# Performance work log

Hardware: AMD Instinct MI355X
Metric: run time of the kernel (lower is better)

The kernel has to match this reference:

```python
import jax, jax.numpy as jnp
import numpy as np

U, G, I, D = 10000, 3000, 8000, 32
LAYERS, SOCIAL_LAYERS = 3, 2
NNZ_UI, NNZ_GI = 720000, 440000
L_MEM = 20
B = 4096


def setup_inputs() -> dict:
    key = jax.random.key(0)
    ks = jax.random.split(key, 24)
    s_u = 1.0 / np.sqrt(U).astype(np.float32)
    s_i = 1.0 / np.sqrt(I).astype(np.float32)
    return {
        "group_inputs": jax.random.randint(ks[0], (B,), 0, G, dtype=jnp.int32),
        "item_inputs": jax.random.randint(ks[1], (B,), 0, I, dtype=jnp.int32),
        "user_emb": jax.random.normal(ks[2], (U, D), jnp.float32) * 0.1,
        "group_emb": jax.random.normal(ks[3], (G, D), jnp.float32) * 0.1,
        "item_emb": jax.random.normal(ks[4], (I, D), jnp.float32) * 0.1,
        "ui_rows": jax.random.randint(ks[5], (NNZ_UI,), 0, U + I, dtype=jnp.int32),
        "ui_cols": jax.random.randint(ks[6], (NNZ_UI,), 0, U + I, dtype=jnp.int32),
        "ui_vals": jax.random.uniform(ks[7], (NNZ_UI,), jnp.float32) * 0.02,
        "gi_rows": jax.random.randint(ks[8], (NNZ_GI,), 0, G + I, dtype=jnp.int32),
        "gi_cols": jax.random.randint(ks[9], (NNZ_GI,), 0, G + I, dtype=jnp.int32),
        "gi_vals": jax.random.uniform(ks[10], (NNZ_GI,), jnp.float32) * 0.02,
        "overlap_user": jax.random.normal(ks[11], (U, U), jnp.float32) * (0.1 * s_u),
        "overlap_item": jax.random.normal(ks[12], (I, I), jnp.float32) * (0.1 * s_i),
        "all_group_users": jax.random.randint(ks[13], (G, L_MEM), 0, U, dtype=jnp.int32),
        "all_group_mask": jax.random.uniform(ks[14], (G, L_MEM), jnp.float32) / L_MEM,
        "gate_w1": jax.random.normal(ks[15], (D, D), jnp.float32) * 0.1,
        "gate_b1": jnp.zeros((D,), jnp.float32),
        "gate_w2": jax.random.normal(ks[16], (D, 1), jnp.float32) * 0.1,
        "gate_b2": jnp.zeros((1,), jnp.float32),
        "pred_w1": jax.random.normal(ks[17], (D, 8), jnp.float32) * 0.1,
        "pred_b1": jnp.zeros((8,), jnp.float32),
        "pred_w2": jax.random.normal(ks[18], (8, 1), jnp.float32) * 0.1,
        "pred_b2": jnp.zeros((1,), jnp.float32),
    }


def _spmm(rows, cols, vals, x, n):
    # COO sparse-dense matmul: out[r] += vals * x[c]
    return jax.ops.segment_sum(vals[:, None] * x[cols], rows, num_segments=n)


def reference(group_inputs, item_inputs, user_emb, group_emb, item_emb,
              ui_rows, ui_cols, ui_vals, gi_rows, gi_cols, gi_vals,
              overlap_user, overlap_item, all_group_users, all_group_mask,
              gate_w1, gate_b1, gate_w2, gate_b2,
              pred_w1, pred_b1, pred_w2, pred_b2):
    # ---- GraphConvolution: user-item propagation ----
    ui = jnp.concatenate([user_emb, item_emb])           # [U+I, D]
    embs_ui = [ui]
    for _ in range(LAYERS):
        ui = _spmm(ui_rows, ui_cols, ui_vals, ui, U + I)
        embs_ui.append(ui)
    user_layers = [e[:U] for e in embs_ui]
    item_layers = [e[U:] for e in embs_ui]
    user_emb_for_user = jnp.mean(jnp.stack(user_layers, 1), axis=1)   # [U, D]
    item_emb_for_user = jnp.mean(jnp.stack(item_layers, 1), axis=1)   # [I, D]

    # ---- group-item propagation ----
    gi = jnp.concatenate([group_emb, item_emb_for_user])  # [G+I, D]
    embs_gi = [gi]
    for _ in range(LAYERS):
        gi = _spmm(gi_rows, gi_cols, gi_vals, gi, G + I)
        embs_gi.append(gi)
    group_gi = [e[:G] for e in embs_gi]
    item_gi = [e[G:] for e in embs_gi]
    i_emb = jnp.mean(jnp.stack(item_gi, 1), axis=1)       # [I, D]

    g_layers = []
    for i in range(LAYERS + 1):
        if i % 2 == 0:
            g_layers.append(group_gi[i])
        else:
            emb_in = jnp.concatenate([group_emb, item_layers[i - 1]])
            g_layers.append(_spmm(gi_rows, gi_cols, gi_vals, emb_in, G + I)[:G])
    g_emb = jnp.mean(jnp.stack(g_layers, 1), axis=1)      # [G, D]

    # ---- SocialRelationshipAgg (dense power-series + gathered pooling) ----
    ue = user_emb_for_user
    acc = ue
    for _ in range(SOCIAL_LAYERS):
        ue = overlap_user @ ue
        acc = acc + ue
    members = acc[all_group_users]                        # [G, L, D]
    group_userlayer = jnp.einsum('gl,gld->gd', all_group_mask, members)

    # ---- Gate ----
    x = jnp.concatenate([g_emb, group_userlayer])         # [2G, D]
    h = jax.nn.relu(x @ gate_w1 + gate_b1)
    w = jax.nn.sigmoid(h @ gate_w2 + gate_b2)             # [2G, 1]
    group_final = w[:G] * g_emb + w[G:] * group_userlayer

    # ---- OverlapGraphConvolution on items ----
    it = i_emb
    iacc = it
    for _ in range(SOCIAL_LAYERS):
        it = overlap_item @ it
        iacc = iacc + it

    # ---- Predict ----
    ge = group_final[group_inputs]                        # [B, D]
    ie = iacc[item_inputs]                                # [B, D]
    p = jax.nn.relu((ge * ie) @ pred_w1 + pred_b1)
    return jax.nn.sigmoid(p @ pred_w2 + pred_b2)          # [B, 1]
```

## Files before the change

### kernel.cpp

```cpp
#include <hip/hip_runtime.h>
#include <math.h>

#define U_N 10000
#define G_N 3000
#define I_N 8000
#define D_N 32
#define NNZ_UI 720000
#define NNZ_GI 440000
#define L_MEM 20
#define B_N 4096
#define UI_N (U_N + I_N)
#define GI_N (G_N + I_N)
#define CAP 128
#define KSPLIT 8

static __host__ int cdiv(int a, int b) { return (a + b - 1) / b; }

typedef __attribute__((ext_vector_type(8))) short bf16x8;
typedef __attribute__((ext_vector_type(4))) float f32x4;

__device__ __forceinline__ short f32_to_bf16(float f) {
    unsigned u = __float_as_uint(f);
    unsigned r = (u + 0x7FFFu + ((u >> 16) & 1u)) >> 16;
    return (short)r;
}


__global__ __launch_bounds__(256) void bucket_fill(const int* __restrict__ rows,
                                                   const int* __restrict__ cols,
                                                   const float* __restrict__ vals,
                                                   int nnz, int* __restrict__ cnt,
                                                   int2* __restrict__ bkt) {
    int i = blockIdx.x * 256 + threadIdx.x;
    if (i >= nnz) return;
    int r = rows[i];
    int pos = atomicAdd(&cnt[r], 1);
    if (pos < CAP) {
        int2 e; e.x = cols[i]; e.y = __float_as_int(vals[i]);
        bkt[(size_t)r * CAP + pos] = e;
    }
}

__global__ __launch_bounds__(256) void spmm_split(const int* __restrict__ cnt,
                                                  const int2* __restrict__ bkt,
                                                  const float* __restrict__ x1,
                                                  const float* __restrict__ x2,
                                                  int split,
                                                  float* __restrict__ out, int nrows) {
    int row = blockIdx.x * 8 + (threadIdx.x >> 5);
    if (row >= nrows) return;
    int d = threadIdx.x & 31;
    int deg = cnt[row];
    if (deg > CAP) deg = CAP;
    const int2* bk = bkt + (size_t)row * CAP;
    float acc = 0.f;
    int j = 0;
#define GATHER(e) ((e.x < split) ? x1[(size_t)e.x * 32 + d] \
                                 : x2[(size_t)(e.x - split) * 32 + d])
    for (; j + 3 < deg; j += 4) {
        int2 e0 = bk[j], e1 = bk[j + 1], e2 = bk[j + 2], e3 = bk[j + 3];
        float g0 = GATHER(e0), g1 = GATHER(e1), g2 = GATHER(e2), g3 = GATHER(e3);
        acc = fmaf(__int_as_float(e0.y), g0, acc);
        acc = fmaf(__int_as_float(e1.y), g1, acc);
        acc = fmaf(__int_as_float(e2.y), g2, acc);
        acc = fmaf(__int_as_float(e3.y), g3, acc);
    }
    for (; j < deg; ++j) {
        int2 e = bk[j];
        acc = fmaf(__int_as_float(e.y), GATHER(e), acc);
    }
#undef GATHER
    out[(size_t)row * 32 + d] = acc;
}


__global__ __launch_bounds__(256) void mean_ui(const float* __restrict__ uemb,
                                               const float* __restrict__ iemb0,
                                               const float* __restrict__ ui1,
                                               const float* __restrict__ ui2,
                                               const float* __restrict__ ui3,
                                               float* __restrict__ uefu,
                                               float* __restrict__ accu,
                                               float* __restrict__ iefu) {
    int idx = blockIdx.x * 256 + threadIdx.x;
    if (idx >= UI_N * 32) return;
    const int UOFF = U_N * 32;
    float base = (idx < UOFF) ? uemb[idx] : iemb0[idx - UOFF];
    float m = 0.25f * (base + ui1[idx] + ui2[idx] + ui3[idx]);
    if (idx < UOFF) { uefu[idx] = m; accu[idx] = m; }
    else iefu[idx - UOFF] = m;
}

__global__ __launch_bounds__(256) void mean_gi_items(const float* __restrict__ iefu,
                                                     const float* __restrict__ gi1,
                                                     const float* __restrict__ gi2,
                                                     const float* __restrict__ gi3,
                                                     float* __restrict__ iemb,
                                                     float* __restrict__ iacc) {
    int idx = blockIdx.x * 256 + threadIdx.x;
    if (idx >= I_N * 32) return;
    const int GOFF = G_N * 32;
    float m = 0.25f * (iefu[idx] + gi1[GOFF + idx] + gi2[GOFF + idx] + gi3[GOFF + idx]);
    iemb[idx] = m;
    iacc[idx] = m;
}

__global__ __launch_bounds__(256) void mean_g(const float* __restrict__ gemb0,
                                              const float* __restrict__ gt1,
                                              const float* __restrict__ gi2,
                                              const float* __restrict__ gt3,
                                              float* __restrict__ gemb) {
    int idx = blockIdx.x * 256 + threadIdx.x;
    if (idx >= G_N * 32) return;
    gemb[idx] = 0.25f * (gemb0[idx] + gt1[idx] + gi2[idx] + gt3[idx]);
}


__global__ __launch_bounds__(256) void pack_xb(const float* __restrict__ x,
                                               short* __restrict__ XB, int N, int ktiles) {
    int idx = blockIdx.x * 256 + threadIdx.x;
    int total = ktiles * 2 * 64;
    if (idx >= total) return;
    int lane = idx & 63;
    int th = idx >> 6;
    int h = th & 1;
    int t = th >> 1;
    int q = lane >> 4;
    int n = (lane & 15) + h * 16;
    short v[8];
#pragma unroll
    for (int j = 0; j < 8; ++j) {
        int c = t * 32 + q * 8 + j;
        v[j] = (c < N) ? f32_to_bf16(x[(size_t)c * 32 + n]) : (short)0;
    }
    short* dst = XB + (size_t)idx * 8;
#pragma unroll
    for (int j = 0; j < 8; ++j) dst[j] = v[j];
}

__global__ __launch_bounds__(256) void dense_mfma(const float* __restrict__ A,
                                                  const short* __restrict__ XB,
                                                  float* __restrict__ out,
                                                  float* __restrict__ out2,
                                                  int N, int ktiles) {
    int wid = (blockIdx.x * 256 + threadIdx.x) >> 6;
    int lane = threadIdx.x & 63;
    int strips = N >> 4;
    int strip = wid / KSPLIT;
    int ks = wid - strip * KSPLIT;
    if (strip >= strips) return;
    int r0 = strip << 4;
    int m = lane & 15;
    int q = lane >> 4;
    const float* arow = A + (size_t)(r0 + m) * N + q * 8;
    const bf16x8* xb = (const bf16x8*)XB;
    f32x4 acc0 = {0.f, 0.f, 0.f, 0.f};
    f32x4 acc1 = {0.f, 0.f, 0.f, 0.f};
    for (int t = ks; t < ktiles; t += KSPLIT) {
        int c0 = t * 32;
        bf16x8 afrag;
        if (c0 + 32 <= N) {
            float4 lo = *(const float4*)(arow + c0);
            float4 hi = *(const float4*)(arow + c0 + 4);
            afrag[0] = f32_to_bf16(lo.x); afrag[1] = f32_to_bf16(lo.y);
            afrag[2] = f32_to_bf16(lo.z); afrag[3] = f32_to_bf16(lo.w);
            afrag[4] = f32_to_bf16(hi.x); afrag[5] = f32_to_bf16(hi.y);
            afrag[6] = f32_to_bf16(hi.z); afrag[7] = f32_to_bf16(hi.w);
        } else {
#pragma unroll
            for (int j = 0; j < 8; ++j) {
                int c = c0 + q * 8 + j;
                afrag[j] = (c < N) ? f32_to_bf16(arow[c0 + j]) : (short)0;
            }
        }
        bf16x8 b0 = xb[(size_t)(t * 2 + 0) * 64 + lane];
        bf16x8 b1 = xb[(size_t)(t * 2 + 1) * 64 + lane];
        acc0 = __builtin_amdgcn_mfma_f32_16x16x32_bf16(afrag, b0, acc0, 0, 0, 0);
        acc1 = __builtin_amdgcn_mfma_f32_16x16x32_bf16(afrag, b1, acc1, 0, 0, 0);
    }
#pragma unroll
    for (int i = 0; i < 4; ++i) {
        size_t o = (size_t)(r0 + q * 4 + i) * 32 + m;
        atomicAdd(&out[o], acc0[i]);
        atomicAdd(&out[o + 16], acc1[i]);
        if (out2) {
            atomicAdd(&out2[o], acc0[i]);
            atomicAdd(&out2[o + 16], acc1[i]);
        }
    }
}

__global__ __launch_bounds__(256) void pool_gate_mix(const int* __restrict__ users,
                                                     const float* __restrict__ mask,
                                                     const float* __restrict__ accu,
                                                     const float* __restrict__ gemb,
                                                     const float* __restrict__ W1,
                                                     const float* __restrict__ b1,
                                                     const float* __restrict__ w2,
                                                     const float* __restrict__ b2,
                                                     float* __restrict__ gfin) {
    int g = blockIdx.x * 8 + (threadIdx.x >> 5);
    if (g >= G_N) return;
    int j = threadIdx.x & 31;
    float gl = 0.f;
#pragma unroll
    for (int l = 0; l < L_MEM; ++l) {
        int u = users[g * L_MEM + l];
        gl = fmaf(mask[g * L_MEM + l], accu[(size_t)u * 32 + j], gl);
    }
    float ge = gemb[(size_t)g * 32 + j];
    float h1 = b1[j], h2 = b1[j];
#pragma unroll
    for (int k = 0; k < 32; ++k) {
        float w = W1[k * 32 + j];
        h1 = fmaf(__shfl(ge, k, 32), w, h1);
        h2 = fmaf(__shfl(gl, k, 32), w, h2);
    }
    float w2j = w2[j];
    float t1 = fmaxf(h1, 0.f) * w2j;
    float t2 = fmaxf(h2, 0.f) * w2j;
#pragma unroll
    for (int off = 16; off >= 1; off >>= 1) {
        t1 += __shfl_xor(t1, off, 32);
        t2 += __shfl_xor(t2, off, 32);
    }
    float bb = b2[0];
    float wa = 1.f / (1.f + expf(-(t1 + bb)));
    float wb = 1.f / (1.f + expf(-(t2 + bb)));
    gfin[(size_t)g * 32 + j] = wa * ge + wb * gl;
}

__global__ __launch_bounds__(256) void predict_kernel(const int* __restrict__ gidx,
                                                      const int* __restrict__ iidx,
                                                      const float* __restrict__ gfin,
                                                      const float* __restrict__ iacc,
                                                      const float* __restrict__ pw1,
                                                      const float* __restrict__ pb1,
                                                      const float* __restrict__ pw2,
                                                      const float* __restrict__ pb2,
                                                      float* __restrict__ out) {
    int b = blockIdx.x * 256 + threadIdx.x;
    if (b >= B_N) return;
    const float* ge = gfin + (size_t)gidx[b] * 32;
    const float* ie = iacc + (size_t)iidx[b] * 32;
    float p[8];
#pragma unroll
    for (int j = 0; j < 8; ++j) p[j] = pb1[j];
    for (int d = 0; d < 32; ++d) {
        float t = ge[d] * ie[d];
#pragma unroll
        for (int j = 0; j < 8; ++j) p[j] = fmaf(t, pw1[d * 8 + j], p[j]);
    }
    float s = pb2[0];
#pragma unroll
    for (int j = 0; j < 8; ++j) s = fmaf(fmaxf(p[j], 0.f), pw2[j], s);
    out[b] = 1.f / (1.f + expf(-s));
}


extern "C" void kernel_launch(void* const* d_in, const int* in_sizes, int n_in,
                              void* d_out, int out_size, void* d_ws, size_t ws_size,
                              hipStream_t stream) {
    const int*   gin   = (const int*)d_in[0];
    const int*   iin   = (const int*)d_in[1];
    const float* uemb  = (const float*)d_in[2];
    const float* gemb0 = (const float*)d_in[3];
    const float* iemb0 = (const float*)d_in[4];
    const int*   uir   = (const int*)d_in[5];
    const int*   uic   = (const int*)d_in[6];
    const float* uiv   = (const float*)d_in[7];
    const int*   gir   = (const int*)d_in[8];
    const int*   gic   = (const int*)d_in[9];
    const float* giv   = (const float*)d_in[10];
    const float* ov_u  = (const float*)d_in[11];
    const float* ov_i  = (const float*)d_in[12];
    const int*   agu   = (const int*)d_in[13];
    const float* agm   = (const float*)d_in[14];
    const float* gw1   = (const float*)d_in[15];
    const float* gb1   = (const float*)d_in[16];
    const float* gw2   = (const float*)d_in[17];
    const float* gb2   = (const float*)d_in[18];
    const float* pw1   = (const float*)d_in[19];
    const float* pb1   = (const float*)d_in[20];
    const float* pw2   = (const float*)d_in[21];
    const float* pb2   = (const float*)d_in[22];
    float* out = (float*)d_out;

    const int KT_U = (U_N + 31) / 32;
    const int KT_I = I_N / 32;

    char* wp = (char*)d_ws;
    auto alloc = [&](size_t nbytes) -> void* {
        void* p = (void*)wp;
        wp += (nbytes + 255) & ~(size_t)255;
        return p;
    };
    int*   cnt_ui = (int*)alloc((size_t)UI_N * 4);
    int*   cnt_gi = (int*)alloc((size_t)GI_N * 4);
    int2*  bkt_ui = (int2*)alloc((size_t)UI_N * CAP * 8);
    int2*  bkt_gi = (int2*)alloc((size_t)GI_N * CAP * 8);
    float* uea  = (float*)alloc((size_t)U_N * 32 * 4);
    float* ita  = (float*)alloc((size_t)I_N * 32 * 4);

    float* ui1  = (float*)alloc((size_t)UI_N * 32 * 4);
    float* ui2  = (float*)alloc((size_t)UI_N * 32 * 4);
    float* ui3  = (float*)alloc((size_t)UI_N * 32 * 4);
    float* gi1  = (float*)alloc((size_t)GI_N * 32 * 4);
    float* gi2  = (float*)alloc((size_t)GI_N * 32 * 4);
    float* gi3  = (float*)alloc((size_t)GI_N * 32 * 4);
    float* uefu = (float*)alloc((size_t)U_N * 32 * 4);
    float* iefu = (float*)alloc((size_t)I_N * 32 * 4);
    float* iemb = (float*)alloc((size_t)I_N * 32 * 4);
    float* gt1  = (float*)alloc((size_t)G_N * 32 * 4);
    float* gt3  = (float*)alloc((size_t)G_N * 32 * 4);
    float* gemb = (float*)alloc((size_t)G_N * 32 * 4);
    float* accu = (float*)alloc((size_t)U_N * 32 * 4);
    float* gfin = (float*)alloc((size_t)G_N * 32 * 4);
    float* iacc = (float*)alloc((size_t)I_N * 32 * 4);
    short* xbu  = (short*)alloc((size_t)KT_U * 2 * 64 * 8 * 2);
    short* xbi  = (short*)alloc((size_t)KT_I * 2 * 64 * 8 * 2);

    hipMemsetAsync(cnt_ui, 0, (size_t)(UI_N + GI_N) * 4 + 256, stream);
    bucket_fill<<<cdiv(NNZ_UI, 256), 256, 0, stream>>>(uir, uic, uiv, NNZ_UI, cnt_ui, bkt_ui);
    bucket_fill<<<cdiv(NNZ_GI, 256), 256, 0, stream>>>(gir, gic, giv, NNZ_GI, cnt_gi, bkt_gi);
    hipMemsetAsync(uea, 0, (size_t)(U_N + I_N) * 32 * 4 + 256, stream);

    spmm_split<<<cdiv(UI_N, 8), 256, 0, stream>>>(cnt_ui, bkt_ui, uemb, iemb0, U_N, ui1, UI_N);
    spmm_split<<<cdiv(UI_N, 8), 256, 0, stream>>>(cnt_ui, bkt_ui, ui1, ui1 + (size_t)U_N * 32, U_N, ui2, UI_N);
    spmm_split<<<cdiv(UI_N, 8), 256, 0, stream>>>(cnt_ui, bkt_ui, ui2, ui2 + (size_t)U_N * 32, U_N, ui3, UI_N);
    mean_ui<<<cdiv(UI_N * 32, 256), 256, 0, stream>>>(uemb, iemb0, ui1, ui2, ui3, uefu, accu, iefu);

    spmm_split<<<cdiv(GI_N, 8), 256, 0, stream>>>(cnt_gi, bkt_gi, gemb0, iefu, G_N, gi1, GI_N);
    spmm_split<<<cdiv(GI_N, 8), 256, 0, stream>>>(cnt_gi, bkt_gi, gi1, gi1 + (size_t)G_N * 32, G_N, gi2, GI_N);
    spmm_split<<<cdiv(GI_N, 8), 256, 0, stream>>>(cnt_gi, bkt_gi, gi2, gi2 + (size_t)G_N * 32, G_N, gi3, GI_N);
    mean_gi_items<<<cdiv(I_N * 32, 256), 256, 0, stream>>>(iefu, gi1, gi2, gi3, iemb, iacc);

    spmm_split<<<cdiv(G_N, 8), 256, 0, stream>>>(cnt_gi, bkt_gi, gemb0, iemb0, G_N, gt1, G_N);
    spmm_split<<<cdiv(G_N, 8), 256, 0, stream>>>(cnt_gi, bkt_gi, gemb0, ui2 + (size_t)U_N * 32, G_N, gt3, G_N);
    mean_g<<<cdiv(G_N * 32, 256), 256, 0, stream>>>(gemb0, gt1, gi2, gt3, gemb);

    const int U_STRIPS = U_N / 16, I_STRIPS = I_N / 16;
    pack_xb<<<cdiv(KT_U * 128, 256), 256, 0, stream>>>(uefu, xbu, U_N, KT_U);
    dense_mfma<<<cdiv(U_STRIPS * KSPLIT, 4), 256, 0, stream>>>(ov_u, xbu, uea, accu, U_N, KT_U);
    pack_xb<<<cdiv(KT_U * 128, 256), 256, 0, stream>>>(uea, xbu, U_N, KT_U);
    dense_mfma<<<cdiv(U_STRIPS * KSPLIT, 4), 256, 0, stream>>>(ov_u, xbu, accu, nullptr, U_N, KT_U);

    pool_gate_mix<<<cdiv(G_N, 8), 256, 0, stream>>>(agu, agm, accu, gemb,
                                                    gw1, gb1, gw2, gb2, gfin);

    pack_xb<<<cdiv(KT_I * 128, 256), 256, 0, stream>>>(iemb, xbi, I_N, KT_I);
    dense_mfma<<<cdiv(I_STRIPS * KSPLIT, 4), 256, 0, stream>>>(ov_i, xbi, ita, iacc, I_N, KT_I);
    pack_xb<<<cdiv(KT_I * 128, 256), 256, 0, stream>>>(ita, xbi, I_N, KT_I);
    dense_mfma<<<cdiv(I_STRIPS * KSPLIT, 4), 256, 0, stream>>>(ov_i, xbi, iacc, nullptr, I_N, KT_I);

    predict_kernel<<<cdiv(B_N, 256), 256, 0, stream>>>(gin, iin, gfin, iacc,
                                                       pw1, pb1, pw2, pb2, out);
}
```

Measured before the change: 1.091 ms.

## Replace atomic split-K reduction with in-block LDS reduction and fuse small kernels

The dense overlap matmul now gives each 16-row strip one 512-thread block whose eight waves split K and reduce through shared memory, instead of global float atomics. The second pass also folds the accumulator add directly into its output. This removes the large memset of the output buffers and the atomic traffic. Separately, the two bucket_fill launches are merged, the two group-only spmm launches are merged into one, and the group mean is folded into pool_gate_mix to cut launch count. Fewer, larger blocks may reduce parallelism on the dense kernel.

```diff
diff --git a/kernel.cpp b/kernel.cpp
--- a/kernel.cpp
+++ b/kernel.cpp
@@ -12,7 +12,6 @@
 #define UI_N (U_N + I_N)
 #define GI_N (G_N + I_N)
 #define CAP 128
-#define KSPLIT 8
 
 static __host__ int cdiv(int a, int b) { return (a + b - 1) / b; }
 
@@ -26,20 +25,39 @@
 }
 
 
-__global__ __launch_bounds__(256) void bucket_fill(const int* __restrict__ rows,
-                                                   const int* __restrict__ cols,
-                                                   const float* __restrict__ vals,
-                                                   int nnz, int* __restrict__ cnt,
-                                                   int2* __restrict__ bkt) {
+__global__ __launch_bounds__(256) void bucket_fill2(const int* __restrict__ uir,
+                                                    const int* __restrict__ uic,
+                                                    const float* __restrict__ uiv,
+                                                    const int* __restrict__ gir,
+                                                    const int* __restrict__ gic,
+                                                    const float* __restrict__ giv,
+                                                    int* __restrict__ cnt_ui,
+                                                    int* __restrict__ cnt_gi,
+                                                    int2* __restrict__ bkt_ui,
+                                                    int2* __restrict__ bkt_gi) {
     int i = blockIdx.x * 256 + threadIdx.x;
-    if (i >= nnz) return;
-    int r = rows[i];
-    int pos = atomicAdd(&cnt[r], 1);
-    if (pos < CAP) {
-        int2 e; e.x = cols[i]; e.y = __float_as_int(vals[i]);
-        bkt[(size_t)r * CAP + pos] = e;
-    }
-}
+    if (i < NNZ_UI) {
+        int r = uir[i];
+        int pos = atomicAdd(&cnt_ui[r], 1);
+        if (pos < CAP) {
+            int2 e; e.x = uic[i]; e.y = __float_as_int(uiv[i]);
+            bkt_ui[(size_t)r * CAP + pos] = e;
+        }
+        return;
+    }
+    int k = i - NNZ_UI;
+    if (k < NNZ_GI) {
+        int r = gir[k];
+        int pos = atomicAdd(&cnt_gi[r], 1);
+        if (pos < CAP) {
+            int2 e; e.x = gic[k]; e.y = __float_as_int(giv[k]);
+            bkt_gi[(size_t)r * CAP + pos] = e;
+        }
+    }
+}
+
+#define GATHER(e) ((e.x < split) ? x1[(size_t)e.x * 32 + d] \
+                                 : x2[(size_t)(e.x - split) * 32 + d])
 
 __global__ __launch_bounds__(256) void spmm_split(const int* __restrict__ cnt,
                                                   const int2* __restrict__ bkt,
@@ -55,8 +73,6 @@
     const int2* bk = bkt + (size_t)row * CAP;
     float acc = 0.f;
     int j = 0;
-#define GATHER(e) ((e.x < split) ? x1[(size_t)e.x * 32 + d] \
-                                 : x2[(size_t)(e.x - split) * 32 + d])
     for (; j + 3 < deg; j += 4) {
         int2 e0 = bk[j], e1 = bk[j + 1], e2 = bk[j + 2], e3 = bk[j + 3];
         float g0 = GATHER(e0), g1 = GATHER(e1), g2 = GATHER(e2), g3 = GATHER(e3);
@@ -69,9 +85,44 @@
         int2 e = bk[j];
         acc = fmaf(__int_as_float(e.y), GATHER(e), acc);
     }
+    out[(size_t)row * 32 + d] = acc;
+}
+
+__global__ __launch_bounds__(256) void spmm_g2(const int* __restrict__ cnt,
+                                               const int2* __restrict__ bkt,
+                                               const float* __restrict__ gemb0,
+                                               const float* __restrict__ iemb0,
+                                               const float* __restrict__ ui2item,
+                                               float* __restrict__ gt1,
+                                               float* __restrict__ gt3) {
+    int row = blockIdx.x * 8 + (threadIdx.x >> 5);
+    if (row >= 2 * G_N) return;
+    int g = (row < G_N) ? row : row - G_N;
+    const float* x1 = gemb0;
+    const float* x2 = (row < G_N) ? iemb0 : ui2item;
+    const int split = G_N;
+    float* out = (row < G_N) ? gt1 : gt3;
+    int d = threadIdx.x & 31;
+    int deg = cnt[g];
+    if (deg > CAP) deg = CAP;
+    const int2* bk = bkt + (size_t)g * CAP;
+    float acc = 0.f;
+    int j = 0;
+    for (; j + 3 < deg; j += 4) {
+        int2 e0 = bk[j], e1 = bk[j + 1], e2 = bk[j + 2], e3 = bk[j + 3];
+        float g0 = GATHER(e0), g1 = GATHER(e1), g2 = GATHER(e2), g3 = GATHER(e3);
+        acc = fmaf(__int_as_float(e0.y), g0, acc);
+        acc = fmaf(__int_as_float(e1.y), g1, acc);
+        acc = fmaf(__int_as_float(e2.y), g2, acc);
+        acc = fmaf(__int_as_float(e3.y), g3, acc);
+    }
+    for (; j < deg; ++j) {
+        int2 e = bk[j];
+        acc = fmaf(__int_as_float(e.y), GATHER(e), acc);
+    }
+    out[(size_t)g * 32 + d] = acc;
+}
 #undef GATHER
-    out[(size_t)row * 32 + d] = acc;
-}
 
 
 __global__ __launch_bounds__(256) void mean_ui(const float* __restrict__ uemb,
@@ -105,16 +156,6 @@
     iacc[idx] = m;
 }
 
-__global__ __launch_bounds__(256) void mean_g(const float* __restrict__ gemb0,
-                                              const float* __restrict__ gt1,
-                                              const float* __restrict__ gi2,
-                                              const float* __restrict__ gt3,
-                                              float* __restrict__ gemb) {
-    int idx = blockIdx.x * 256 + threadIdx.x;
-    if (idx >= G_N * 32) return;
-    gemb[idx] = 0.25f * (gemb0[idx] + gt1[idx] + gi2[idx] + gt3[idx]);
-}
-
 
 __global__ __launch_bounds__(256) void pack_xb(const float* __restrict__ x,
                                                short* __restrict__ XB, int N, int ktiles) {
@@ -138,25 +179,23 @@
     for (int j = 0; j < 8; ++j) dst[j] = v[j];
 }
 
-__global__ __launch_bounds__(256) void dense_mfma(const float* __restrict__ A,
-                                                  const short* __restrict__ XB,
-                                                  float* __restrict__ out,
-                                                  float* __restrict__ out2,
-                                                  int N, int ktiles) {
-    int wid = (blockIdx.x * 256 + threadIdx.x) >> 6;
-    int lane = threadIdx.x & 63;
-    int strips = N >> 4;
-    int strip = wid / KSPLIT;
-    int ks = wid - strip * KSPLIT;
-    if (strip >= strips) return;
-    int r0 = strip << 4;
+__global__ __launch_bounds__(512) void dense_mfma_b(const float* __restrict__ A,
+                                                    const short* __restrict__ XB,
+                                                    float* __restrict__ out,
+                                                    const float* __restrict__ add1,
+                                                    int N, int ktiles) {
+    __shared__ float red[8 * 512];
+    int tid = threadIdx.x;
+    int w = tid >> 6;
+    int lane = tid & 63;
+    int r0 = blockIdx.x << 4;
     int m = lane & 15;
     int q = lane >> 4;
     const float* arow = A + (size_t)(r0 + m) * N + q * 8;
     const bf16x8* xb = (const bf16x8*)XB;
     f32x4 acc0 = {0.f, 0.f, 0.f, 0.f};
     f32x4 acc1 = {0.f, 0.f, 0.f, 0.f};
-    for (int t = ks; t < ktiles; t += KSPLIT) {
+    for (int t = w; t < ktiles; t += 8) {
         int c0 = t * 32;
         bf16x8 afrag;
         if (c0 + 32 <= N) {
@@ -178,22 +217,29 @@
         acc0 = __builtin_amdgcn_mfma_f32_16x16x32_bf16(afrag, b0, acc0, 0, 0, 0);
         acc1 = __builtin_amdgcn_mfma_f32_16x16x32_bf16(afrag, b1, acc1, 0, 0, 0);
     }
+    float* my = red + w * 512;
 #pragma unroll
     for (int i = 0; i < 4; ++i) {
-        size_t o = (size_t)(r0 + q * 4 + i) * 32 + m;
-        atomicAdd(&out[o], acc0[i]);
-        atomicAdd(&out[o + 16], acc1[i]);
-        if (out2) {
-            atomicAdd(&out2[o], acc0[i]);
-            atomicAdd(&out2[o + 16], acc1[i]);
-        }
-    }
+        my[(q * 4 + i) * 32 + m]      = acc0[i];
+        my[(q * 4 + i) * 32 + m + 16] = acc1[i];
+    }
+    __syncthreads();
+    float s = red[tid];
+#pragma unroll
+    for (int wv = 1; wv < 8; ++wv) s += red[wv * 512 + tid];
+    int row = tid >> 5;
+    int col = tid & 31;
+    size_t o = (size_t)(r0 + row) * 32 + col;
+    out[o] = add1 ? (out[o] + add1[o] + s) : s;
 }
 
 __global__ __launch_bounds__(256) void pool_gate_mix(const int* __restrict__ users,
                                                      const float* __restrict__ mask,
                                                      const float* __restrict__ accu,
-                                                     const float* __restrict__ gemb,
+                                                     const float* __restrict__ gemb0,
+                                                     const float* __restrict__ gt1,
+                                                     const float* __restrict__ gi2,
+                                                     const float* __restrict__ gt3,
                                                      const float* __restrict__ W1,
                                                      const float* __restrict__ b1,
                                                      const float* __restrict__ w2,
@@ -202,13 +248,14 @@
     int g = blockIdx.x * 8 + (threadIdx.x >> 5);
     if (g >= G_N) return;
     int j = threadIdx.x & 31;
+    size_t gj = (size_t)g * 32 + j;
+    float ge = 0.25f * (gemb0[gj] + gt1[gj] + gi2[gj] + gt3[gj]);
     float gl = 0.f;
 #pragma unroll
     for (int l = 0; l < L_MEM; ++l) {
         int u = users[g * L_MEM + l];
         gl = fmaf(mask[g * L_MEM + l], accu[(size_t)u * 32 + j], gl);
     }
-    float ge = gemb[(size_t)g * 32 + j];
     float h1 = b1[j], h2 = b1[j];
 #pragma unroll
     for (int k = 0; k < 32; ++k) {
@@ -227,7 +274,7 @@
     float bb = b2[0];
     float wa = 1.f / (1.f + expf(-(t1 + bb)));
     float wb = 1.f / (1.f + expf(-(t2 + bb)));
-    gfin[(size_t)g * 32 + j] = wa * ge + wb * gl;
+    gfin[gj] = wa * ge + wb * gl;
 }
 
 __global__ __launch_bounds__(256) void predict_kernel(const int* __restrict__ gidx,
@@ -297,11 +344,12 @@
     };
     int*   cnt_ui = (int*)alloc((size_t)UI_N * 4);
     int*   cnt_gi = (int*)alloc((size_t)GI_N * 4);
+    size_t zbytes = (size_t)(wp - (char*)cnt_ui);
+
     int2*  bkt_ui = (int2*)alloc((size_t)UI_N * CAP * 8);
     int2*  bkt_gi = (int2*)alloc((size_t)GI_N * CAP * 8);
     float* uea  = (float*)alloc((size_t)U_N * 32 * 4);
     float* ita  = (float*)alloc((size_t)I_N * 32 * 4);
-
     float* ui1  = (float*)alloc((size_t)UI_N * 32 * 4);
     float* ui2  = (float*)alloc((size_t)UI_N * 32 * 4);
     float* ui3  = (float*)alloc((size_t)UI_N * 32 * 4);
@@ -313,21 +361,21 @@
     float* iemb = (float*)alloc((size_t)I_N * 32 * 4);
     float* gt1  = (float*)alloc((size_t)G_N * 32 * 4);
     float* gt3  = (float*)alloc((size_t)G_N * 32 * 4);
-    float* gemb = (float*)alloc((size_t)G_N * 32 * 4);
     float* accu = (float*)alloc((size_t)U_N * 32 * 4);
     float* gfin = (float*)alloc((size_t)G_N * 32 * 4);
     float* iacc = (float*)alloc((size_t)I_N * 32 * 4);
     short* xbu  = (short*)alloc((size_t)KT_U * 2 * 64 * 8 * 2);
     short* xbi  = (short*)alloc((size_t)KT_I * 2 * 64 * 8 * 2);
 
-    hipMemsetAsync(cnt_ui, 0, (size_t)(UI_N + GI_N) * 4 + 256, stream);
-    bucket_fill<<<cdiv(NNZ_UI, 256), 256, 0, stream>>>(uir, uic, uiv, NNZ_UI, cnt_ui, bkt_ui);
-    bucket_fill<<<cdiv(NNZ_GI, 256), 256, 0, stream>>>(gir, gic, giv, NNZ_GI, cnt_gi, bkt_gi);
-    hipMemsetAsync(uea, 0, (size_t)(U_N + I_N) * 32 * 4 + 256, stream);
+    (void)hipMemsetAsync(cnt_ui, 0, zbytes, stream);
+    bucket_fill2<<<cdiv(NNZ_UI + NNZ_GI, 256), 256, 0, stream>>>(
+        uir, uic, uiv, gir, gic, giv, cnt_ui, cnt_gi, bkt_ui, bkt_gi);
 
     spmm_split<<<cdiv(UI_N, 8), 256, 0, stream>>>(cnt_ui, bkt_ui, uemb, iemb0, U_N, ui1, UI_N);
     spmm_split<<<cdiv(UI_N, 8), 256, 0, stream>>>(cnt_ui, bkt_ui, ui1, ui1 + (size_t)U_N * 32, U_N, ui2, UI_N);
     spmm_split<<<cdiv(UI_N, 8), 256, 0, stream>>>(cnt_ui, bkt_ui, ui2, ui2 + (size_t)U_N * 32, U_N, ui3, UI_N);
+    spmm_g2<<<cdiv(2 * G_N, 8), 256, 0, stream>>>(cnt_gi, bkt_gi, gemb0, iemb0,
+                                                  ui2 + (size_t)U_N * 32, gt1, gt3);
     mean_ui<<<cdiv(UI_N * 32, 256), 256, 0, stream>>>(uemb, iemb0, ui1, ui2, ui3, uefu, accu, iefu);
 
     spmm_split<<<cdiv(GI_N, 8), 256, 0, stream>>>(cnt_gi, bkt_gi, gemb0, iefu, G_N, gi1, GI_N);
@@ -335,23 +383,19 @@
     spmm_split<<<cdiv(GI_N, 8), 256, 0, stream>>>(cnt_gi, bkt_gi, gi2, gi2 + (size_t)G_N * 32, G_N, gi3, GI_N);
     mean_gi_items<<<cdiv(I_N * 32, 256), 256, 0, stream>>>(iefu, gi1, gi2, gi3, iemb, iacc);
 
-    spmm_split<<<cdiv(G_N, 8), 256, 0, stream>>>(cnt_gi, bkt_gi, gemb0, iemb0, G_N, gt1, G_N);
-    spmm_split<<<cdiv(G_N, 8), 256, 0, stream>>>(cnt_gi, bkt_gi, gemb0, ui2 + (size_t)U_N * 32, G_N, gt3, G_N);
-    mean_g<<<cdiv(G_N * 32, 256), 256, 0, stream>>>(gemb0, gt1, gi2, gt3, gemb);
-
     const int U_STRIPS = U_N / 16, I_STRIPS = I_N / 16;
     pack_xb<<<cdiv(KT_U * 128, 256), 256, 0, stream>>>(uefu, xbu, U_N, KT_U);
-    dense_mfma<<<cdiv(U_STRIPS * KSPLIT, 4), 256, 0, stream>>>(ov_u, xbu, uea, accu, U_N, KT_U);
+    dense_mfma_b<<<U_STRIPS, 512, 0, stream>>>(ov_u, xbu, uea, nullptr, U_N, KT_U);
     pack_xb<<<cdiv(KT_U * 128, 256), 256, 0, stream>>>(uea, xbu, U_N, KT_U);
-    dense_mfma<<<cdiv(U_STRIPS * KSPLIT, 4), 256, 0, stream>>>(ov_u, xbu, accu, nullptr, U_N, KT_U);
-
-    pool_gate_mix<<<cdiv(G_N, 8), 256, 0, stream>>>(agu, agm, accu, gemb,
+    dense_mfma_b<<<U_STRIPS, 512, 0, stream>>>(ov_u, xbu, accu, uea, U_N, KT_U);
+
+    pool_gate_mix<<<cdiv(G_N, 8), 256, 0, stream>>>(agu, agm, accu, gemb0, gt1, gi2, gt3,
                                                     gw1, gb1, gw2, gb2, gfin);
 
     pack_xb<<<cdiv(KT_I * 128, 256), 256, 0, stream>>>(iemb, xbi, I_N, KT_I);
-    dense_mfma<<<cdiv(I_STRIPS * KSPLIT, 4), 256, 0, stream>>>(ov_i, xbi, ita, iacc, I_N, KT_I);
+    dense_mfma_b<<<I_STRIPS, 512, 0, stream>>>(ov_i, xbi, ita, nullptr, I_N, KT_I);
     pack_xb<<<cdiv(KT_I * 128, 256), 256, 0, stream>>>(ita, xbi, I_N, KT_I);
-    dense_mfma<<<cdiv(I_STRIPS * KSPLIT, 4), 256, 0, stream>>>(ov_i, xbi, iacc, nullptr, I_N, KT_I);
+    dense_mfma_b<<<I_STRIPS, 512, 0, stream>>>(ov_i, xbi, iacc, ita, I_N, KT_I);
 
     predict_kernel<<<cdiv(B_N, 256), 256, 0, stream>>>(gin, iin, gfin, iacc,
                                                        pw1, pb1, pw2, pb2, out);
```

Result: no change. 1.106 ms (+1.4%).
